# Kernel optimization log

Measured on AMD Instinct MI355X. Metric: run time of the kernel, lower is better.

The kernel has to match this reference:

```python
import jax, jax.numpy as jnp
import numpy as np

NUM_EXPERTS = 64
HIDDEN_DIM = 4096
TOPK = 8


def setup_inputs() -> dict:
    key = jax.random.key(0)
    kx, kw = jax.random.split(key)
    x = jax.random.normal(kx, (16384, HIDDEN_DIM), dtype=jnp.float32)
    # nn.Linear weight is [num_experts, hidden_dim], init N(0, 0.01)
    W = jax.random.normal(kw, (NUM_EXPERTS, HIDDEN_DIM), dtype=jnp.float32) * 0.01
    return {"x": x, "W": W}


def reference(x, W):
    # router logits: [T, E]
    router_logits = jnp.einsum('th,eh->te', x, W)
    score = jnp.clip(router_logits, -2.0, 2.0)
    # top-k over experts (no router_bias branch)
    topk_scores, topk_indices = jax.lax.top_k(score, TOPK)  # [T, K]
    topk_probs = jax.nn.softmax(topk_scores, axis=-1)
    # dispatch index computation (counting-sort style)
    flat = topk_indices.reshape(-1)                      # [T*K]
    indices = jnp.argsort(flat, stable=True).astype(jnp.int32)
    tokens_per_expert = jnp.bincount(flat, length=NUM_EXPERTS)
    group_indices = jnp.cumsum(tokens_per_expert).astype(jnp.int32)
    tokens_per_expert_f = tokens_per_expert.astype(jnp.float32)
    # load-balance loss
    mean_tokens = tokens_per_expert_f / tokens_per_expert_f.sum()
    mean_prob = jax.nn.softmax(router_logits, axis=-1).mean(axis=0)
    lb_loss = jnp.dot(mean_tokens, mean_prob) * NUM_EXPERTS
    # z-loss
    zl = jnp.mean(jax.scipy.special.logsumexp(router_logits, axis=-1) ** 2)
    return (router_logits, topk_probs, topk_indices, group_indices,
            indices, tokens_per_expert, lb_loss, zl)
```

## Files before the change

kernel.cpp:

```cpp
#include <hip/hip_runtime.h>
#include <hip/hip_bf16.h>
#include <math.h>

#define NTOK   16384
#define NEXP   64
#define HID    4096
#define KSEL   8
#define EPS    7.5e-5f
#define NSPLIT 4
#define KSZ    (HID / NSPLIT)

typedef __attribute__((ext_vector_type(8))) short short8;
typedef __attribute__((ext_vector_type(4))) float f32x4;

#define O_LOGITS 0u
#define O_PROBS  1048576u
#define O_TIDX   1179648u
#define O_GROUP  1310720u
#define O_IDX    1310784u
#define O_TPE    1441856u
#define O_LB     1441920u
#define O_ZL     1441921u

#define W_CQ      0u
#define W_LSQP    8192u
#define W_PSUM    81920u
#define W_FLAT    262144u
#define W_WF      1048576u
#define W_PART    2097152u
#define PART_STRIDE 1048576ull

__device__ __forceinline__ unsigned short f2bf(float f) {
  unsigned u = __float_as_uint(f);
  return (unsigned short)((u + 0x7fffu + ((u >> 16) & 1u)) >> 16);
}

__device__ __forceinline__ void gload16(const void* g, void* l) {
  __builtin_amdgcn_global_load_lds((const __attribute__((address_space(1))) unsigned int*)g,
                                   (__attribute__((address_space(3))) unsigned int*)l, 16, 0, 0);
}

__global__ __launch_bounds__(256) void k_prep(const float* __restrict__ w,
                                              short8* __restrict__ wf,
                                              int* __restrict__ cq) {
  const int kk   = blockIdx.x;
  const int nb   = threadIdx.x >> 6;
  const int lane = threadIdx.x & 63;
  const int n    = nb * 16 + (lane & 15);
  const int kb   = kk * 32 + (lane >> 4) * 8;
  const float4* wp = (const float4*)(w + (size_t)n * HID + kb);
  float4 f0 = wp[0], f1 = wp[1];
  float fv[8] = {f0.x, f0.y, f0.z, f0.w, f1.x, f1.y, f1.z, f1.w};
  short8 hi, lo;
#pragma unroll
  for (int j = 0; j < 8; ++j) {
    unsigned short h = f2bf(fv[j]);
    hi[j] = (short)h;
    float r = fv[j] - __uint_as_float((unsigned)h << 16);
    lo[j] = (short)f2bf(r);
  }
  size_t base = ((size_t)(kk * 4 + nb) * 2) * 64 + lane;
  wf[base] = hi;
  wf[base + 64] = lo;
  if (blockIdx.x == 0) {
    cq[threadIdx.x] = 0;
    cq[threadIdx.x + 256] = 0;
  }
}

__global__ __launch_bounds__(256, 4) void k_gemm(const float* __restrict__ x,
                                                 const short8* __restrict__ wf,
                                                 float* __restrict__ part) {
  __shared__ short8 wl[2][512];
  const int tid  = threadIdx.x;
  const int wv   = tid >> 6;
  const int lane = tid & 63;
  const int t0   = blockIdx.x * 64;
  const int k0   = blockIdx.y * KSZ;
  const int row  = t0 + wv * 16 + (lane & 15);

  const float* xp = x + (size_t)row * HID + k0 + (lane >> 4) * 8;
  const short8* wbase = wf + (size_t)(k0 >> 5) * 512;

  auto stage = [&](int c, int b) {
    const short8* src = wbase + (size_t)c * 512;
#pragma unroll
    for (int r = 0; r < 2; ++r) {
      const int o = r * 256 + wv * 64;
      gload16(src + o + lane, &wl[b][o]);
    }
  };

  f32x4 acc[4] = {{0,0,0,0},{0,0,0,0},{0,0,0,0},{0,0,0,0}};

  stage(0, 0);
  __syncthreads();
  const int nch = KSZ >> 5;
  for (int c = 0; c < nch; ++c) {
    const int b = c & 1;
    if (c + 1 < nch) stage(c + 1, b ^ 1);

    const float4* xq = (const float4*)(xp + c * 32);
    float4 f0 = xq[0], f1 = xq[1];
    unsigned xb[8] = {__float_as_uint(f0.x), __float_as_uint(f0.y),
                      __float_as_uint(f0.z), __float_as_uint(f0.w),
                      __float_as_uint(f1.x), __float_as_uint(f1.y),
                      __float_as_uint(f1.z), __float_as_uint(f1.w)};
    union { unsigned u[4]; short8 s; } ua, ul;
#pragma unroll
    for (int p = 0; p < 4; ++p) {
      unsigned b0 = xb[2 * p], b1 = xb[2 * p + 1];
      ua.u[p] = __builtin_amdgcn_perm(b1, b0, 0x07060302u);
      float r0 = __uint_as_float(b0) - __uint_as_float(b0 & 0xffff0000u);
      float r1 = __uint_as_float(b1) - __uint_as_float(b1 & 0xffff0000u);
      unsigned t0b = __float_as_uint(r0), t1b = __float_as_uint(r1);
      t0b += 0x7fffu + ((t0b >> 16) & 1u);
      t1b += 0x7fffu + ((t1b >> 16) & 1u);
      ul.u[p] = __builtin_amdgcn_perm(t1b, t0b, 0x07060302u);
    }
    short8 ah = ua.s, al = ul.s;

#pragma unroll
    for (int nb = 0; nb < 4; ++nb) {
      short8 bh = wl[b][nb * 128 + lane];
      short8 bl = wl[b][nb * 128 + 64 + lane];
      acc[nb] = __builtin_amdgcn_mfma_f32_16x16x32_bf16(ah, bh, acc[nb], 0, 0, 0);
      acc[nb] = __builtin_amdgcn_mfma_f32_16x16x32_bf16(al, bh, acc[nb], 0, 0, 0);
      acc[nb] = __builtin_amdgcn_mfma_f32_16x16x32_bf16(ah, bl, acc[nb], 0, 0, 0);
    }
    __syncthreads();
  }

  float* p = part + (size_t)blockIdx.y * PART_STRIDE;
  const int mrow = t0 + wv * 16 + (lane >> 4) * 4;
  const int col  = lane & 15;
#pragma unroll
  for (int nb = 0; nb < 4; ++nb)
#pragma unroll
    for (int r = 0; r < 4; ++r)
      p[(size_t)(mrow + r) * 64 + nb * 16 + col] = acc[nb][r];
}

__global__ __launch_bounds__(256) void k_reduce(const float* __restrict__ part,
                                                float* __restrict__ out_logits) {
  unsigned i4 = blockIdx.x * 256u + threadIdx.x;
  const float4* p4 = (const float4*)part;
  float4 v = p4[i4];
#pragma unroll
  for (int s = 1; s < NSPLIT; ++s) {
    float4 a = p4[(size_t)s * (PART_STRIDE / 4) + i4];
    v.x += a.x; v.y += a.y; v.z += a.z; v.w += a.w;
  }
  ((float4*)out_logits)[i4] = v;
}

__global__ __launch_bounds__(256) void k_rowwise(const float* __restrict__ lg,
                                                 const float* __restrict__ x,
                                                 const float* __restrict__ w,
                                                 float* __restrict__ out,
                                                 int* __restrict__ cq,
                                                 float* __restrict__ psum,
                                                 float* __restrict__ lsqp,
                                                 int* __restrict__ flat) {
  __shared__ float tile[64][68];
  __shared__ float rmv[64], invv[64], val8s[64];
  __shared__ int   hist[64];
  __shared__ int   fl_rows[64];
  __shared__ int   fl_n;
  __shared__ unsigned long long candmask;
  __shared__ double cexact[64];
  const int bid  = blockIdx.x;
  const int tid  = threadIdx.x;
  const int wv   = tid >> 6;
  const int lane = tid & 63;
  const int t0   = bid * 64;
  if (tid < 64) hist[tid] = 0;
  if (tid == 0) fl_n = 0;

  {
    const size_t boff = (size_t)bid * 4096;
#pragma unroll
    for (int k = 0; k < 16; ++k) {
      int idx = k * 256 + tid;
      tile[idx >> 6][idx & 63] = lg[boff + idx];
    }
  }
  __syncthreads();

  if (wv == 1) {
    const int r = lane;
    float rm = -3.0e38f;
#pragma unroll
    for (int c4 = 0; c4 < 16; ++c4) {
      float4 f = *(float4*)&tile[r][c4 * 4];
      rm = fmaxf(rm, fmaxf(fmaxf(f.x, f.y), fmaxf(f.z, f.w)));
    }
    float se = 0.0f;
#pragma unroll
    for (int c4 = 0; c4 < 16; ++c4) {
      float4 f = *(float4*)&tile[r][c4 * 4];
      se += expf(f.x - rm) + expf(f.y - rm) + expf(f.z - rm) + expf(f.w - rm);
    }
    rmv[r] = rm; invv[r] = 1.0f / se;
    float lse = rm + logf(se);
    float l2 = lse * lse;
#pragma unroll
    for (int o = 32; o > 0; o >>= 1) l2 += __shfl_down(l2, o);
    if (lane == 0) lsqp[bid] = l2;
  }
  __syncthreads();

  if (wv == 0) {
    const unsigned t = t0 + lane;
    float val[9]; int idx[9];
#pragma unroll
    for (int j = 0; j < 9; ++j) { val[j] = -3.0e38f; idx[j] = 0; }
    bool flag = false;
#pragma unroll
    for (int c4 = 0; c4 < 16; ++c4) {
      float4 f = *(float4*)&tile[lane][c4 * 4];
      float fe[4] = {f.x, f.y, f.z, f.w};
#pragma unroll
      for (int jj = 0; jj < 4; ++jj) {
        float v = fe[jj];
        flag = flag || (fabsf(fabsf(v) - 2.0f) < EPS);
        float c = fminf(fmaxf(v, -2.0f), 2.0f);
        int id = c4 * 4 + jj;
#pragma unroll
        for (int j = 0; j < 9; ++j) {
          bool sw = c > val[j];
          float tv = sw ? val[j] : c; int ti = sw ? idx[j] : id;
          val[j] = sw ? c : val[j];   idx[j] = sw ? id : idx[j];
          c = tv; id = ti;
        }
      }
    }
    val8s[lane] = val[8];
#pragma unroll
    for (int j = 0; j < 8; ++j) {
      float gap = val[j] - val[j + 1];
      bool bothclip = (val[j] == val[j + 1]) && (fabsf(val[j]) == 2.0f);
      flag = flag || (gap < EPS && !bothclip);
    }
    if (!flag) {
      float m = val[0], pe[8], sum = 0.0f;
#pragma unroll
      for (int j = 0; j < 8; ++j) { pe[j] = expf(val[j] - m); sum += pe[j]; }
      float inv = 1.0f / sum;
      *(float4*)&out[O_PROBS + (size_t)t * 8]     = make_float4(pe[0]*inv, pe[1]*inv, pe[2]*inv, pe[3]*inv);
      *(float4*)&out[O_PROBS + (size_t)t * 8 + 4] = make_float4(pe[4]*inv, pe[5]*inv, pe[6]*inv, pe[7]*inv);
      *(float4*)&out[O_TIDX + (size_t)t * 8]      = make_float4((float)idx[0], (float)idx[1], (float)idx[2], (float)idx[3]);
      *(float4*)&out[O_TIDX + (size_t)t * 8 + 4]  = make_float4((float)idx[4], (float)idx[5], (float)idx[6], (float)idx[7]);
      *(int4*)&flat[(size_t)t * 8]     = make_int4(idx[0], idx[1], idx[2], idx[3]);
      *(int4*)&flat[(size_t)t * 8 + 4] = make_int4(idx[4], idx[5], idx[6], idx[7]);
#pragma unroll
      for (int j = 0; j < 8; ++j) atomicAdd(&hist[idx[j]], 1);
    } else {
      int sl = atomicAdd(&fl_n, 1);
      fl_rows[sl] = lane;
    }
  } else if (wv == 2 || wv == 3) {
    const int e = lane, half = wv - 2;
    float s = 0.0f;
#pragma unroll
    for (int r = 0; r < 32; ++r) {
      int rr = half * 32 + r;
      s += expf(tile[rr][e] - rmv[rr]) * invv[rr];
    }
    psum[(size_t)bid * 128 + half * 64 + e] = s;
  }
  __syncthreads();

  for (int i = 0; i < fl_n; ++i) {
    const int r = fl_rows[i];
    if (wv == 0) {
      float c = fminf(fmaxf(tile[r][lane], -2.0f), 2.0f);
      bool cnd = (c >= val8s[r] - 3.0f * EPS);
      unsigned long long m = __ballot(cnd);
      if (lane == 0) candmask = m;
    }
    __syncthreads();
    const unsigned long long m = candmask;
    const float* xr = x + (size_t)(t0 + r) * HID;
    {
      int ord = 0;
      for (int e = 0; e < 64; ++e) {
        if ((m >> e) & 1ull) {
          if ((ord & 3) == wv) {
            const float* wr = w + (size_t)e * HID;
            double p0 = 0.0, p1 = 0.0, p2 = 0.0, p3 = 0.0;
            const int kb = lane * 64;
            for (int k = kb; k < kb + 64; k += 4) {
              float4 xv = *(const float4*)&xr[k];
              float4 wv4 = *(const float4*)&wr[k];
              p0 = fma((double)xv.x, (double)wv4.x, p0);
              p1 = fma((double)xv.y, (double)wv4.y, p1);
              p2 = fma((double)xv.z, (double)wv4.z, p2);
              p3 = fma((double)xv.w, (double)wv4.w, p3);
            }
            double p = (p0 + p1) + (p2 + p3);
#pragma unroll
            for (int o = 32; o > 0; o >>= 1) p += __shfl_down(p, o);
            if (lane == 0) cexact[e] = fmin(fmax(p, -2.0), 2.0);
          }
          ord++;
        }
      }
    }
    __syncthreads();
    if (tid == r) {
      double val[8]; int idx[8];
#pragma unroll
      for (int j = 0; j < 8; ++j) { val[j] = -1.0e300; idx[j] = 0; }
      for (int e = 0; e < 64; ++e) {
        if (!((m >> e) & 1ull)) continue;
        double c = cexact[e];
        int id = e;
#pragma unroll
        for (int j = 0; j < 8; ++j) {
          bool sw = c > val[j];
          double tv = sw ? val[j] : c; int ti = sw ? idx[j] : id;
          val[j] = sw ? c : val[j];    idx[j] = sw ? id : idx[j];
          c = tv; id = ti;
        }
      }
      float mm = (float)val[0], pe[8], sum = 0.0f;
#pragma unroll
      for (int j = 0; j < 8; ++j) { pe[j] = expf((float)val[j] - mm); sum += pe[j]; }
      float inv = 1.0f / sum;
      const unsigned t = t0 + r;
#pragma unroll
      for (int j = 0; j < 8; ++j) {
        out[O_PROBS + (size_t)t * 8 + j] = pe[j] * inv;
        out[O_TIDX  + (size_t)t * 8 + j] = (float)idx[j];
        flat[(size_t)t * 8 + j] = idx[j];
        atomicAdd(&hist[idx[j]], 1);
      }
    }
    __syncthreads();
  }

  if (tid < 64) atomicAdd(&cq[(bid >> 5) * 64 + tid], hist[tid]);
}

__global__ __launch_bounds__(256) void k_dispatch(const int* __restrict__ flat,
                                                  const int* __restrict__ cq,
                                                  const float* __restrict__ psum,
                                                  const float* __restrict__ lsqp,
                                                  float* __restrict__ out) {
  __shared__ int ctot[64];
  __shared__ int sbase;
  __shared__ int wcs[4];
  __shared__ float gsum[4][64];
  const int e = blockIdx.x >> 3;
  const int q = blockIdx.x & 7;
  const int tid = threadIdx.x;
  const int lane = tid & 63;
  const int wv = tid >> 6;

  if (tid < 64) {
    int tpe = 0;
#pragma unroll
    for (int qq = 0; qq < 8; ++qq) tpe += cq[qq * 64 + tid];
    ctot[tid] = tpe;
  }
  __syncthreads();
  if (tid == 0) {
    int b = 0;
    for (int i = 0; i < e; ++i) b += ctot[i];
    for (int qq = 0; qq < q; ++qq) b += cq[qq * 64 + e];
    sbase = b;
  }

  if (blockIdx.x == 0) {
    const int e2 = tid & 63, g = tid >> 6;
    float ps = 0.0f;
    for (int b = g; b < 256; b += 4) ps += psum[(size_t)b * 128 + e2] + psum[(size_t)b * 128 + 64 + e2];
    gsum[g][e2] = ps;
    __syncthreads();
    if (tid < 64) {
      int incl = 0;
      for (int i = 0; i <= tid; ++i) incl += ctot[i];
      int tpe = ctot[tid];
      out[O_TPE + tid]   = (float)tpe;
      out[O_GROUP + tid] = (float)incl;
      float pst = (gsum[0][tid] + gsum[1][tid]) + (gsum[2][tid] + gsum[3][tid]);
      float term = ((float)tpe / 131072.0f) * (pst / 16384.0f) * 64.0f;
#pragma unroll
      for (int o2 = 32; o2 > 0; o2 >>= 1) term += __shfl_down(term, o2);
      float zs = (lsqp[tid * 4] + lsqp[tid * 4 + 1]) + (lsqp[tid * 4 + 2] + lsqp[tid * 4 + 3]);
#pragma unroll
      for (int o2 = 32; o2 > 0; o2 >>= 1) zs += __shfl_down(zs, o2);
      if (tid == 0) { out[O_LB] = term; out[O_ZL] = zs / 16384.0f; }
    }
  }
  __syncthreads();

  int base = sbase;
  const int seg0 = q * 16384;
  for (int c0 = 0; c0 < 16384; c0 += 2048) {
    const int j0 = seg0 + c0 + tid * 8;
    const int4* f4 = reinterpret_cast<const int4*>(flat + j0);
    int4 a = f4[0], b = f4[1];
    int v[8] = {a.x, a.y, a.z, a.w, b.x, b.y, b.z, b.w};
    int mcnt = 0;
#pragma unroll
    for (int k = 0; k < 8; ++k) mcnt += (v[k] == e) ? 1 : 0;
    int sc = mcnt;
#pragma unroll
    for (int o = 1; o < 64; o <<= 1) {
      int nn = __shfl_up(sc, o);
      if (lane >= o) sc += nn;
    }
    int excl = sc - mcnt;
    if (lane == 63) wcs[wv] = sc;
    __syncthreads();
    int woff = 0, tot = 0;
#pragma unroll
    for (int i = 0; i < 4; ++i) { int ci = wcs[i]; woff += (i < wv) ? ci : 0; tot += ci; }
    int pos = base + woff + excl;
#pragma unroll
    for (int k = 0; k < 8; ++k) {
      if (v[k] == e) { out[O_IDX + pos] = (float)(j0 + k); pos++; }
    }
    base += tot;
    __syncthreads();
  }
}

extern "C" void kernel_launch(void* const* d_in, const int* in_sizes, int n_in,
                              void* d_out, int out_size, void* d_ws, size_t ws_size,
                              hipStream_t stream) {
  (void)in_sizes; (void)n_in; (void)out_size; (void)ws_size;
  const float* x  = (const float*)d_in[0];
  const float* Wm = (const float*)d_in[1];
  float* out = (float*)d_out;
  char*  ws  = (char*)d_ws;

  int*    cq     = (int*)(ws + W_CQ);
  float*  lsqp   = (float*)(ws + W_LSQP);
  float*  psum   = (float*)(ws + W_PSUM);
  int*    flat   = (int*)(ws + W_FLAT);
  short8* wf     = (short8*)(ws + W_WF);
  float*  part   = (float*)(ws + W_PART);

  k_prep    <<<dim3(128), dim3(256), 0, stream>>>(Wm, wf, cq);
  k_gemm    <<<dim3(NTOK / 64, NSPLIT), dim3(256), 0, stream>>>(x, wf, part);
  k_reduce  <<<dim3(1024), dim3(256), 0, stream>>>(part, out + O_LOGITS);
  k_rowwise <<<dim3(256), dim3(256), 0, stream>>>(out + O_LOGITS, x, Wm, out, cq, psum, lsqp, flat);
  k_dispatch<<<dim3(512), dim3(256), 0, stream>>>(flat, cq, psum, lsqp, out);
}
```

Baseline: 157.0 us.

## Replace per-expert dispatch scan with per-block rank plus global scatter

Builds the stable counting-sort dispatch differently. Each rowwise block now computes a within-block rank and per-expert counts in LDS. A single-block scan kernel then forms per-block, per-expert prefix offsets, and a flat scatter kernel writes each index directly. This removes the old dispatch kernel, where each of 512 blocks rescanned 16384 flat entries for one expert. The cost is an extra launch, a serial 256-step scan on 64 threads, and a serial per-wave ranking loop in LDS.

```diff
diff --git a/kernel.cpp b/kernel.cpp
--- a/kernel.cpp
+++ b/kernel.cpp
@@ -22,12 +22,14 @@
 #define O_LB     1441920u
 #define O_ZL     1441921u
 
-#define W_CQ      0u
-#define W_LSQP    8192u
-#define W_PSUM    81920u
-#define W_FLAT    262144u
-#define W_WF      1048576u
-#define W_PART    2097152u
+#define W_LSQP    4096u
+#define W_CBE     8192u
+#define W_PREF    73728u
+#define W_PSUM    262144u
+#define W_FLAT    524288u
+#define W_RNK     1048576u
+#define W_WF      2097152u
+#define W_PART    4194304u
 #define PART_STRIDE 1048576ull
 
 __device__ __forceinline__ unsigned short f2bf(float f) {
@@ -41,8 +43,7 @@
 }
 
 __global__ __launch_bounds__(256) void k_prep(const float* __restrict__ w,
-                                              short8* __restrict__ wf,
-                                              int* __restrict__ cq) {
+                                              short8* __restrict__ wf) {
   const int kk   = blockIdx.x;
   const int nb   = threadIdx.x >> 6;
   const int lane = threadIdx.x & 63;
@@ -62,10 +63,6 @@
   size_t base = ((size_t)(kk * 4 + nb) * 2) * 64 + lane;
   wf[base] = hi;
   wf[base + 64] = lo;
-  if (blockIdx.x == 0) {
-    cq[threadIdx.x] = 0;
-    cq[threadIdx.x + 256] = 0;
-  }
 }
 
 __global__ __launch_bounds__(256, 4) void k_gemm(const float* __restrict__ x,
@@ -158,13 +155,16 @@
                                                  const float* __restrict__ x,
                                                  const float* __restrict__ w,
                                                  float* __restrict__ out,
-                                                 int* __restrict__ cq,
                                                  float* __restrict__ psum,
                                                  float* __restrict__ lsqp,
-                                                 int* __restrict__ flat) {
+                                                 int* __restrict__ flat,
+                                                 int* __restrict__ rnk_g,
+                                                 int* __restrict__ cbe) {
   __shared__ float tile[64][68];
   __shared__ float rmv[64], invv[64], val8s[64];
-  __shared__ int   hist[64];
+  __shared__ int   ids[512];
+  __shared__ int   rnk_lds[512];
+  __shared__ int   cntq[4][64];
   __shared__ int   fl_rows[64];
   __shared__ int   fl_n;
   __shared__ unsigned long long candmask;
@@ -174,7 +174,6 @@
   const int wv   = tid >> 6;
   const int lane = tid & 63;
   const int t0   = bid * 64;
-  if (tid < 64) hist[tid] = 0;
   if (tid == 0) fl_n = 0;
 
   {
@@ -254,7 +253,7 @@
       *(int4*)&flat[(size_t)t * 8]     = make_int4(idx[0], idx[1], idx[2], idx[3]);
       *(int4*)&flat[(size_t)t * 8 + 4] = make_int4(idx[4], idx[5], idx[6], idx[7]);
 #pragma unroll
-      for (int j = 0; j < 8; ++j) atomicAdd(&hist[idx[j]], 1);
+      for (int j = 0; j < 8; ++j) ids[lane * 8 + j] = idx[j];
     } else {
       int sl = atomicAdd(&fl_n, 1);
       fl_rows[sl] = lane;
@@ -334,98 +333,85 @@
         out[O_PROBS + (size_t)t * 8 + j] = pe[j] * inv;
         out[O_TIDX  + (size_t)t * 8 + j] = (float)idx[j];
         flat[(size_t)t * 8 + j] = idx[j];
-        atomicAdd(&hist[idx[j]], 1);
+        ids[r * 8 + j] = idx[j];
       }
     }
     __syncthreads();
   }
 
-  if (tid < 64) atomicAdd(&cq[(bid >> 5) * 64 + tid], hist[tid]);
-}
-
-__global__ __launch_bounds__(256) void k_dispatch(const int* __restrict__ flat,
-                                                  const int* __restrict__ cq,
-                                                  const float* __restrict__ psum,
-                                                  const float* __restrict__ lsqp,
-                                                  float* __restrict__ out) {
+  {
+    int cnt = 0;
+    const int base = wv * 128;
+    for (int i = base; i < base + 128; ++i) {
+      int id = ids[i];
+      if (id == lane) { rnk_lds[i] = cnt; cnt++; }
+    }
+    cntq[wv][lane] = cnt;
+  }
+  __syncthreads();
+
+#pragma unroll
+  for (int k2 = 0; k2 < 2; ++k2) {
+    const int i = tid * 2 + k2;
+    const int e = ids[i];
+    int r = rnk_lds[i];
+    const int q = i >> 7;
+    for (int wq = 0; wq < q; ++wq) r += cntq[wq][e];
+    rnk_g[(size_t)bid * 512 + i] = r;
+  }
+  if (tid < 64)
+    cbe[bid * 64 + tid] = cntq[0][tid] + cntq[1][tid] + cntq[2][tid] + cntq[3][tid];
+}
+
+__global__ __launch_bounds__(256) void k_scan(const int* __restrict__ cbe,
+                                              const float* __restrict__ psum,
+                                              const float* __restrict__ lsqp,
+                                              int* __restrict__ pref,
+                                              float* __restrict__ out) {
   __shared__ int ctot[64];
-  __shared__ int sbase;
-  __shared__ int wcs[4];
   __shared__ float gsum[4][64];
-  const int e = blockIdx.x >> 3;
-  const int q = blockIdx.x & 7;
   const int tid = threadIdx.x;
-  const int lane = tid & 63;
-  const int wv = tid >> 6;
+  const int e = tid & 63, g = tid >> 6;
+
+  float ps = 0.0f;
+  for (int b = g; b < 256; b += 4) ps += psum[(size_t)b * 128 + e] + psum[(size_t)b * 128 + 64 + e];
+  gsum[g][e] = ps;
 
   if (tid < 64) {
-    int tpe = 0;
-#pragma unroll
-    for (int qq = 0; qq < 8; ++qq) tpe += cq[qq * 64 + tid];
-    ctot[tid] = tpe;
-  }
-  __syncthreads();
-  if (tid == 0) {
-    int b = 0;
-    for (int i = 0; i < e; ++i) b += ctot[i];
-    for (int qq = 0; qq < q; ++qq) b += cq[qq * 64 + e];
-    sbase = b;
-  }
-
-  if (blockIdx.x == 0) {
-    const int e2 = tid & 63, g = tid >> 6;
-    float ps = 0.0f;
-    for (int b = g; b < 256; b += 4) ps += psum[(size_t)b * 128 + e2] + psum[(size_t)b * 128 + 64 + e2];
-    gsum[g][e2] = ps;
-    __syncthreads();
-    if (tid < 64) {
-      int incl = 0;
-      for (int i = 0; i <= tid; ++i) incl += ctot[i];
-      int tpe = ctot[tid];
-      out[O_TPE + tid]   = (float)tpe;
-      out[O_GROUP + tid] = (float)incl;
-      float pst = (gsum[0][tid] + gsum[1][tid]) + (gsum[2][tid] + gsum[3][tid]);
-      float term = ((float)tpe / 131072.0f) * (pst / 16384.0f) * 64.0f;
-#pragma unroll
-      for (int o2 = 32; o2 > 0; o2 >>= 1) term += __shfl_down(term, o2);
-      float zs = (lsqp[tid * 4] + lsqp[tid * 4 + 1]) + (lsqp[tid * 4 + 2] + lsqp[tid * 4 + 3]);
-#pragma unroll
-      for (int o2 = 32; o2 > 0; o2 >>= 1) zs += __shfl_down(zs, o2);
-      if (tid == 0) { out[O_LB] = term; out[O_ZL] = zs / 16384.0f; }
-    }
-  }
-  __syncthreads();
-
-  int base = sbase;
-  const int seg0 = q * 16384;
-  for (int c0 = 0; c0 < 16384; c0 += 2048) {
-    const int j0 = seg0 + c0 + tid * 8;
-    const int4* f4 = reinterpret_cast<const int4*>(flat + j0);
-    int4 a = f4[0], b = f4[1];
-    int v[8] = {a.x, a.y, a.z, a.w, b.x, b.y, b.z, b.w};
-    int mcnt = 0;
-#pragma unroll
-    for (int k = 0; k < 8; ++k) mcnt += (v[k] == e) ? 1 : 0;
-    int sc = mcnt;
-#pragma unroll
-    for (int o = 1; o < 64; o <<= 1) {
-      int nn = __shfl_up(sc, o);
-      if (lane >= o) sc += nn;
-    }
-    int excl = sc - mcnt;
-    if (lane == 63) wcs[wv] = sc;
-    __syncthreads();
-    int woff = 0, tot = 0;
-#pragma unroll
-    for (int i = 0; i < 4; ++i) { int ci = wcs[i]; woff += (i < wv) ? ci : 0; tot += ci; }
-    int pos = base + woff + excl;
-#pragma unroll
-    for (int k = 0; k < 8; ++k) {
-      if (v[k] == e) { out[O_IDX + pos] = (float)(j0 + k); pos++; }
-    }
-    base += tot;
-    __syncthreads();
-  }
+    int s = 0;
+    for (int b = 0; b < 256; ++b) s += cbe[b * 64 + tid];
+    ctot[tid] = s;
+  }
+  __syncthreads();
+
+  if (tid < 64) {
+    int incl = 0;
+    for (int i = 0; i <= tid; ++i) incl += ctot[i];
+    const int tpe = ctot[tid];
+    out[O_TPE + tid]   = (float)tpe;
+    out[O_GROUP + tid] = (float)incl;
+    int run = incl - tpe;
+    for (int b = 0; b < 256; ++b) { pref[b * 64 + tid] = run; run += cbe[b * 64 + tid]; }
+
+    float pst = (gsum[0][tid] + gsum[1][tid]) + (gsum[2][tid] + gsum[3][tid]);
+    float term = ((float)tpe / 131072.0f) * (pst / 16384.0f) * 64.0f;
+#pragma unroll
+    for (int o2 = 32; o2 > 0; o2 >>= 1) term += __shfl_down(term, o2);
+    float zs = (lsqp[tid * 4] + lsqp[tid * 4 + 1]) + (lsqp[tid * 4 + 2] + lsqp[tid * 4 + 3]);
+#pragma unroll
+    for (int o2 = 32; o2 > 0; o2 >>= 1) zs += __shfl_down(zs, o2);
+    if (tid == 0) { out[O_LB] = term; out[O_ZL] = zs / 16384.0f; }
+  }
+}
+
+__global__ __launch_bounds__(256) void k_scatter(const int* __restrict__ flat,
+                                                 const int* __restrict__ rnk,
+                                                 const int* __restrict__ pref,
+                                                 float* __restrict__ out) {
+  const int j = blockIdx.x * 256 + threadIdx.x;
+  const int e = flat[j];
+  const int pos = pref[(j >> 9) * 64 + e] + rnk[j];
+  out[O_IDX + pos] = (float)j;
 }
 
 extern "C" void kernel_launch(void* const* d_in, const int* in_sizes, int n_in,
@@ -437,16 +423,19 @@
   float* out = (float*)d_out;
   char*  ws  = (char*)d_ws;
 
-  int*    cq     = (int*)(ws + W_CQ);
   float*  lsqp   = (float*)(ws + W_LSQP);
+  int*    cbe    = (int*)(ws + W_CBE);
+  int*    pref   = (int*)(ws + W_PREF);
   float*  psum   = (float*)(ws + W_PSUM);
   int*    flat   = (int*)(ws + W_FLAT);
+  int*    rnk    = (int*)(ws + W_RNK);
   short8* wf     = (short8*)(ws + W_WF);
   float*  part   = (float*)(ws + W_PART);
 
-  k_prep    <<<dim3(128), dim3(256), 0, stream>>>(Wm, wf, cq);
-  k_gemm    <<<dim3(NTOK / 64, NSPLIT), dim3(256), 0, stream>>>(x, wf, part);
-  k_reduce  <<<dim3(1024), dim3(256), 0, stream>>>(part, out + O_LOGITS);
-  k_rowwise <<<dim3(256), dim3(256), 0, stream>>>(out + O_LOGITS, x, Wm, out, cq, psum, lsqp, flat);
-  k_dispatch<<<dim3(512), dim3(256), 0, stream>>>(flat, cq, psum, lsqp, out);
-}
+  k_prep   <<<dim3(128),  dim3(256), 0, stream>>>(Wm, wf);
+  k_gemm   <<<dim3(NTOK / 64, NSPLIT), dim3(256), 0, stream>>>(x, wf, part);
+  k_reduce <<<dim3(1024), dim3(256), 0, stream>>>(part, out + O_LOGITS);
+  k_rowwise<<<dim3(256),  dim3(256), 0, stream>>>(out + O_LOGITS, x, Wm, out, psum, lsqp, flat, rnk, cbe);
+  k_scan   <<<dim3(1),    dim3(256), 0, stream>>>(cbe, psum, lsqp, pref, out);
+  k_scatter<<<dim3(512),  dim3(256), 0, stream>>>(flat, rnk, pref, out);
+}
```

Result: slower. 170.3 us (+8.4%).
